# Kernel optimization log

Hardware: AMD Instinct MI355X
Metric: run time of the kernel (lower is better)

## Reference

```python
import jax, jax.numpy as jnp
import numpy as np

B, C, F = 262144, 64, 256
N_ITERS = 8


def setup_inputs() -> dict:
    key = jax.random.key(0)
    ks = jax.random.split(key, 8)
    s = lambda fan_in: 1.0 / np.sqrt(fan_in)
    return {
        "y": jax.random.normal(ks[0], (B, C), jnp.float32),
        "log_det_jacobians": jnp.zeros((B,), jnp.float32),
        "v": jax.random.normal(ks[1], (B, 1, C), jnp.float32),
        "W1": jax.random.normal(ks[2], (F, C), jnp.float32) * s(C),
        "b1": jnp.zeros((F,), jnp.float32),
        "W2": jax.random.normal(ks[3], (F, F), jnp.float32) * s(F),
        "b2": jnp.zeros((F,), jnp.float32),
        "W3": jax.random.normal(ks[4], (C, F), jnp.float32) * s(F),
        "b3": jnp.zeros((C,), jnp.float32),
    }


def reference(y, log_det_jacobians, v, W1, b1, W2, b2, W3, b3):
    def mlp(t):
        h = jax.nn.elu(t)
        h = jax.nn.elu(h @ W1.T + b1)
        h = jax.nn.elu(h @ W2.T + b2)
        return h @ W3.T + b3  # [B, C]

    g_y, vjp_fn = jax.vjp(mlp, y)
    v0 = v[:, 0, :]  # n_samples = 1
    w = v0
    log_det = jnp.zeros((y.shape[0],), y.dtype)
    for k in range(1, N_ITERS + 1):
        w = vjp_fn(w)[0]              # w <- w @ J, J = dg/dy
        inner = jnp.einsum('bd,bd->b', w, v0)
        # torch code: add when (k+1) % 2 == 0 (k odd), subtract when k even
        log_det = log_det + (inner / k if (k + 1) % 2 == 0 else -inner / k)

    z = y + g_y
    return z, log_det_jacobians + log_det
```

## Files before the change

kernel.cpp:

```cpp
#include <hip/hip_runtime.h>

#define BN 262144

typedef short bf16x8 __attribute__((ext_vector_type(8)));
typedef float f32x4 __attribute__((ext_vector_type(4)));
typedef unsigned int u32x2 __attribute__((ext_vector_type(2)));

#define MFMA16(a,b,c) __builtin_amdgcn_mfma_f32_16x16x32_bf16((a),(b),(c),0,0,0)

__device__ __forceinline__ unsigned short f2bf(float f) {
  union { float f; unsigned int u; } x; x.f = f;
  unsigned int u = x.u + 0x7fffu + ((x.u >> 16) & 1u);
  return (unsigned short)(u >> 16);
}
__device__ __forceinline__ float bf2f(unsigned int h) {
  union { unsigned int u; float f; } x; x.u = h << 16;
  return x.f;
}
__device__ __forceinline__ unsigned pk2(float lo, float hi) {
  union { float f; unsigned int u; } a, b; a.f = lo; b.f = hi;
  return (a.u >> 16) | (b.u & 0xffff0000u);
}
__device__ __forceinline__ unsigned swz(int row) {
  return (((unsigned)(row & 7)) << 4) ^ (((unsigned)(row & 8)) << 2);
}

#define O_R1 0
#define O_R2 16384
#define O_R3 81920
#define O_R4 98304
#define O_R5 114688
#define O_R6 180224
#define N_WS 196608

__global__ void invres_prep(const float* __restrict__ W1, const float* __restrict__ W2,
                            const float* __restrict__ W3, unsigned short* __restrict__ wsb) {
  int idx = blockIdx.x * 256 + threadIdx.x;
  if (idx >= N_WS) return;
  int j = idx & 7;
  int lane = (idx >> 3) & 63;
  int nn = lane & 15, kn = (lane >> 4) * 8 + j;
  float val;
  if (idx < O_R2) {
    int g = idx >> 9; int s = g & 1; int ct = g >> 1;
    val = W1[(ct * 16 + nn) * 64 + (s * 32 + kn)];
  } else if (idx < O_R3) {
    int g = (idx - O_R2) >> 9; int s = g & 7; int ct = g >> 3;
    val = W2[(ct * 16 + nn) * 256 + (s * 32 + kn)];
  } else if (idx < O_R4) {
    int g = (idx - O_R3) >> 9; int s = g & 7; int ct = g >> 3;
    val = W3[(ct * 16 + nn) * 256 + (s * 32 + kn)];
  } else if (idx < O_R5) {
    int g = (idx - O_R4) >> 9; int s = g & 1; int ct = g >> 1;
    val = W3[(s * 32 + kn) * 256 + (ct * 16 + nn)];
  } else if (idx < O_R6) {
    int g = (idx - O_R5) >> 9; int s = g & 7; int ct = g >> 3;
    val = W2[(s * 32 + kn) * 256 + (ct * 16 + nn)];
  } else {
    int g = (idx - O_R6) >> 9; int s = g & 7; int ct = g >> 3;
    val = W1[(s * 32 + kn) * 64 + (ct * 16 + nn)];
  }
  wsb[idx] = f2bf(val);
}

#define L_WB  16384
#define L_D1  20480
#define L_D2  36864
#define L_LDP 53248
#define L_SIZE 53760

__global__ void __launch_bounds__(512, 6)
invres_main(const float* __restrict__ y, const float* __restrict__ ldj,
            const float* __restrict__ v, const float* __restrict__ b1,
            const float* __restrict__ b2, const float* __restrict__ b3,
            const unsigned short* __restrict__ wsb, float* __restrict__ out) {
  extern __shared__ char smem[];
  char* P  = smem;
  char* WB = smem + L_WB;
  char* D1 = smem + L_D1;
  char* D2 = smem + L_D2;
  float* ldp = (float*)(smem + L_LDP);

  const int tid = threadIdx.x;
  const int lane = tid & 63;
  const int wid = tid >> 6;
  const int l15 = lane & 15, g16 = lane >> 4;
  const int ct0 = wid * 2;
  const int mh = wid >> 2;
  const int ctn = wid & 3;
  const int r0 = blockIdx.x * 32;

  const bf16x8* R1 = (const bf16x8*)(wsb + O_R1);
  const bf16x8* R2 = (const bf16x8*)(wsb + O_R2);
  const bf16x8* R3 = (const bf16x8*)(wsb + O_R3);
  const bf16x8* R4 = (const bf16x8*)(wsb + O_R4);
  const bf16x8* R5 = (const bf16x8*)(wsb + O_R5);
  const bf16x8* R6 = (const bf16x8*)(wsb + O_R6);

  auto mOff = [&](int mc) -> int { return ((wid * 4 + mc) * 64 + lane) * 8; };

  auto ldsA = [&](const char* buf, int mm, int s) -> bf16x8 {
    int row = mm * 16 + l15;
    unsigned byte = ((unsigned)(s * 64 + g16 * 16)) ^ swz(row);
    return *(const bf16x8*)(buf + row * 512 + byte);
  };
  auto stage64 = [&](char* buf, int mm, int cc, const float* hv) {
    int row = mm * 16 + l15;
    unsigned byte = ((unsigned)(((ct0 + cc) * 16 + g16 * 4) * 2)) ^ swz(row);
    u32x2 w; w[0] = pk2(hv[0], hv[1]); w[1] = pk2(hv[2], hv[3]);
    *(u32x2*)(buf + row * 512 + byte) = w;
  };
  auto gA = [&](const float* p, int mm, int s, bool elu) -> bf16x8 {
    const float* q = p + (size_t)(r0 + mm * 16 + l15) * 64 + s * 32 + g16 * 8;
    f32x4 a = __builtin_nontemporal_load((const f32x4*)q);
    f32x4 b = __builtin_nontemporal_load((const f32x4*)(q + 4));
    float xv[8] = {a[0], a[1], a[2], a[3], b[0], b[1], b[2], b[3]};
    bf16x8 f;
#pragma unroll
    for (int i = 0; i < 8; i++) {
      float x = xv[i];
      if (elu) x = x > 0.f ? x : (__expf(x) - 1.f);
      f[i] = (short)f2bf(x);
    }
    return f;
  };

  unsigned d0p[2], v0p[2];
  float ldacc[4] = {0.f, 0.f, 0.f, 0.f};

  {
    f32x4 bv1[2];
#pragma unroll
    for (int cc = 0; cc < 2; cc++) bv1[cc] = *(const f32x4*)(b1 + (ct0 + cc) * 16 + g16 * 4);
    f32x4 acc[2][2] = {};
#pragma unroll
    for (int s = 0; s < 2; s++) {
      bf16x8 a0 = gA(y, 0, s, true);
      bf16x8 a1 = gA(y, 1, s, true);
#pragma unroll
      for (int cc = 0; cc < 2; cc++) {
        bf16x8 B = R1[((ct0 + cc) * 2 + s) * 64 + lane];
        acc[0][cc] = MFMA16(B, a0, acc[0][cc]);
        acc[1][cc] = MFMA16(B, a1, acc[1][cc]);
      }
    }
#pragma unroll
    for (int mm = 0; mm < 2; mm++)
#pragma unroll
      for (int cc = 0; cc < 2; cc++) {
        float hv[4], dv[4];
#pragma unroll
        for (int r = 0; r < 4; r++) {
          float a = acc[mm][cc][r] + bv1[cc][r];
          float e = __expf(a);
          hv[r] = a > 0.f ? a : (e - 1.f);
          dv[r] = a > 0.f ? 1.f : e;
        }
        stage64(P, mm, cc, hv);
        u32x2 w; w[0] = pk2(dv[0], dv[1]); w[1] = pk2(dv[2], dv[3]);
        *(u32x2*)(D1 + mOff(mm * 2 + cc)) = w;
      }
  }
  __syncthreads();

  {
    f32x4 acc[2][2] = {};
#pragma unroll 1
    for (int s = 0; s < 8; s++) {
      bf16x8 a0 = ldsA(P, 0, s);
      bf16x8 a1 = ldsA(P, 1, s);
      bf16x8 B0 = R2[(ct0 * 8 + s) * 64 + lane];
      bf16x8 B1 = R2[((ct0 + 1) * 8 + s) * 64 + lane];
      acc[0][0] = MFMA16(B0, a0, acc[0][0]);
      acc[0][1] = MFMA16(B1, a0, acc[0][1]);
      acc[1][0] = MFMA16(B0, a1, acc[1][0]);
      acc[1][1] = MFMA16(B1, a1, acc[1][1]);
    }
    __syncthreads();
    f32x4 bv2[2];
#pragma unroll
    for (int cc = 0; cc < 2; cc++) bv2[cc] = *(const f32x4*)(b2 + (ct0 + cc) * 16 + g16 * 4);
#pragma unroll
    for (int mm = 0; mm < 2; mm++)
#pragma unroll
      for (int cc = 0; cc < 2; cc++) {
        float hv[4], dv[4];
#pragma unroll
        for (int r = 0; r < 4; r++) {
          float a = acc[mm][cc][r] + bv2[cc][r];
          float e = __expf(a);
          hv[r] = a > 0.f ? a : (e - 1.f);
          dv[r] = a > 0.f ? 1.f : e;
        }
        stage64(P, mm, cc, hv);
        u32x2 w; w[0] = pk2(dv[0], dv[1]); w[1] = pk2(dv[2], dv[3]);
        *(u32x2*)(D2 + mOff(mm * 2 + cc)) = w;
      }
  }
  __syncthreads();

  {
    f32x4 acc0 = {}, acc1 = {};
#pragma unroll 1
    for (int s = 0; s < 8; s += 2) {
      acc0 = MFMA16(R3[(ctn * 8 + s) * 64 + lane], ldsA(P, mh, s), acc0);
      acc1 = MFMA16(R3[(ctn * 8 + s + 1) * 64 + lane], ldsA(P, mh, s + 1), acc1);
    }
    f32x4 bv3 = *(const f32x4*)(b3 + ctn * 16 + g16 * 4);
    int row = r0 + mh * 16 + l15;
    int col = ctn * 16 + g16 * 4;
    size_t off = (size_t)row * 64 + col;
    f32x4 yv = __builtin_nontemporal_load((const f32x4*)(y + off));
    f32x4 vv = __builtin_nontemporal_load((const f32x4*)(v + off));
    f32x4 zv;
    float d0v[4];
#pragma unroll
    for (int r = 0; r < 4; r++) {
      zv[r] = yv[r] + acc0[r] + acc1[r] + bv3[r];
      d0v[r] = yv[r] > 0.f ? 1.f : __expf(yv[r]);
    }
    __builtin_nontemporal_store(zv, (f32x4*)(out + off));
    d0p[0] = pk2(d0v[0], d0v[1]); d0p[1] = pk2(d0v[2], d0v[3]);
    v0p[0] = pk2(vv[0], vv[1]);   v0p[1] = pk2(vv[2], vv[3]);
  }
  __syncthreads();

  {
    f32x4 acc[2][2] = {};
#pragma unroll
    for (int s = 0; s < 2; s++) {
      bf16x8 a0 = gA(v, 0, s, false);
      bf16x8 a1 = gA(v, 1, s, false);
#pragma unroll
      for (int cc = 0; cc < 2; cc++) {
        bf16x8 B = R4[((ct0 + cc) * 2 + s) * 64 + lane];
        acc[0][cc] = MFMA16(B, a0, acc[0][cc]);
        acc[1][cc] = MFMA16(B, a1, acc[1][cc]);
      }
    }
#pragma unroll
    for (int mm = 0; mm < 2; mm++)
#pragma unroll
      for (int cc = 0; cc < 2; cc++) {
        u32x2 dd = *(const u32x2*)(D2 + mOff(mm * 2 + cc));
        float uv[4];
#pragma unroll
        for (int r = 0; r < 4; r++)
          uv[r] = acc[mm][cc][r] * bf2f((dd[r >> 1] >> ((r & 1) * 16)) & 0xffffu);
        stage64(P, mm, cc, uv);
      }
  }
  __syncthreads();

  for (int k = 1; k <= 8; ++k) {
    {
      f32x4 acc[2][2] = {};
#pragma unroll 1
      for (int s = 0; s < 8; s++) {
        bf16x8 a0 = ldsA(P, 0, s);
        bf16x8 a1 = ldsA(P, 1, s);
        bf16x8 B0 = R5[(ct0 * 8 + s) * 64 + lane];
        bf16x8 B1 = R5[((ct0 + 1) * 8 + s) * 64 + lane];
        acc[0][0] = MFMA16(B0, a0, acc[0][0]);
        acc[0][1] = MFMA16(B1, a0, acc[0][1]);
        acc[1][0] = MFMA16(B0, a1, acc[1][0]);
        acc[1][1] = MFMA16(B1, a1, acc[1][1]);
      }
      __syncthreads();
#pragma unroll
      for (int mm = 0; mm < 2; mm++)
#pragma unroll
        for (int cc = 0; cc < 2; cc++) {
          u32x2 dd = *(const u32x2*)(D1 + mOff(mm * 2 + cc));
          float uv[4];
#pragma unroll
          for (int r = 0; r < 4; r++)
            uv[r] = acc[mm][cc][r] * bf2f((dd[r >> 1] >> ((r & 1) * 16)) & 0xffffu);
          stage64(P, mm, cc, uv);
        }
    }
    __syncthreads();

    {
      float coef = (k & 1) ? (1.f / (float)k) : (-1.f / (float)k);
      f32x4 acc0 = {}, acc1 = {};
#pragma unroll 1
      for (int s = 0; s < 8; s += 2) {
        acc0 = MFMA16(R6[(ctn * 8 + s) * 64 + lane], ldsA(P, mh, s), acc0);
        acc1 = MFMA16(R6[(ctn * 8 + s + 1) * 64 + lane], ldsA(P, mh, s + 1), acc1);
      }
      float wv[4];
#pragma unroll
      for (int r = 0; r < 4; r++) {
        wv[r] = (acc0[r] + acc1[r]) * bf2f((d0p[r >> 1] >> ((r & 1) * 16)) & 0xffffu);
        ldacc[r] += coef * wv[r] * bf2f((v0p[r >> 1] >> ((r & 1) * 16)) & 0xffffu);
      }
      if (k < 8) {
        int row = mh * 16 + l15;
        unsigned byte = ((unsigned)((ctn * 16 + g16 * 4) * 2)) ^ swz(row);
        u32x2 w; w[0] = pk2(wv[0], wv[1]); w[1] = pk2(wv[2], wv[3]);
        *(u32x2*)(WB + row * 128 + byte) = w;
      }
    }
    if (k < 8) {
      __syncthreads();
      f32x4 acc[2][2] = {};
#pragma unroll
      for (int s = 0; s < 2; s++) {
        bf16x8 a0, a1;
#pragma unroll
        for (int mm = 0; mm < 2; mm++) {
          int row = mm * 16 + l15;
          unsigned byte = ((unsigned)(s * 64 + g16 * 16)) ^ swz(row);
          bf16x8 a = *(const bf16x8*)(WB + row * 128 + byte);
          if (mm == 0) a0 = a; else a1 = a;
        }
#pragma unroll
        for (int cc = 0; cc < 2; cc++) {
          bf16x8 B = R4[((ct0 + cc) * 2 + s) * 64 + lane];
          acc[0][cc] = MFMA16(B, a0, acc[0][cc]);
          acc[1][cc] = MFMA16(B, a1, acc[1][cc]);
        }
      }
#pragma unroll
      for (int mm = 0; mm < 2; mm++)
#pragma unroll
        for (int cc = 0; cc < 2; cc++) {
          u32x2 dd = *(const u32x2*)(D2 + mOff(mm * 2 + cc));
          float uv[4];
#pragma unroll
          for (int r = 0; r < 4; r++)
            uv[r] = acc[mm][cc][r] * bf2f((dd[r >> 1] >> ((r & 1) * 16)) & 0xffffu);
          stage64(P, mm, cc, uv);
        }
      __syncthreads();
    }
  }

  {
    float s = ldacc[0] + ldacc[1] + ldacc[2] + ldacc[3];
    s += __shfl_xor(s, 16);
    s += __shfl_xor(s, 32);
    if (g16 == 0) ldp[(mh * 16 + l15) * 4 + ctn] = s;
  }
  __syncthreads();
  if (tid < 32) {
    float s = ldp[tid * 4] + ldp[tid * 4 + 1] + ldp[tid * 4 + 2] + ldp[tid * 4 + 3];
    int gb = r0 + tid;
    __builtin_nontemporal_store(ldj[gb] + s, out + (size_t)BN * 64 + gb);
  }
}

extern "C" void kernel_launch(void* const* d_in, const int* in_sizes, int n_in,
                              void* d_out, int out_size, void* d_ws, size_t ws_size,
                              hipStream_t stream) {
  const float* y   = (const float*)d_in[0];
  const float* ldj = (const float*)d_in[1];
  const float* v   = (const float*)d_in[2];
  const float* W1  = (const float*)d_in[3];
  const float* b1  = (const float*)d_in[4];
  const float* W2  = (const float*)d_in[5];
  const float* b2  = (const float*)d_in[6];
  const float* W3  = (const float*)d_in[7];
  const float* b3  = (const float*)d_in[8];
  unsigned short* wsb = (unsigned short*)d_ws;
  float* out = (float*)d_out;

  (void)hipFuncSetAttribute(reinterpret_cast<const void*>(&invres_main),
                            hipFuncAttributeMaxDynamicSharedMemorySize, L_SIZE);

  invres_prep<<<N_WS / 256, 256, 0, stream>>>(W1, W2, W3, wsb);
  invres_main<<<BN / 32, 512, L_SIZE, stream>>>(y, ldj, v, b1, b2, b3, wsb, out);
}
```

Before: 781.6 us.

## Double-buffer LDS activations and keep ELU derivatives in registers

Replaces the single LDS activation buffer with two ping-pong buffers, PA and PB, so each GEMM reads one buffer while writing the other. This removes the __syncthreads that sat between the MFMA loop and the staging writes in several stages. The bf16-packed ELU derivative masks D1 and D2 move from LDS into per-thread registers (16 extra VGPRs), which removes their LDS traffic and shrinks shared memory use. The cost is more register pressure under launch bounds of 512 threads with 6 blocks, which could force spills.

Measured after the change: 1.376 ms. 1.76x slower.

```diff
diff --git a/kernel.cpp b/kernel.cpp
--- a/kernel.cpp
+++ b/kernel.cpp
@@ -63,11 +63,10 @@
   wsb[idx] = f2bf(val);
 }
 
-#define L_WB  16384
-#define L_D1  20480
-#define L_D2  36864
-#define L_LDP 53248
-#define L_SIZE 53760
+#define L_PB  16384
+#define L_WB  32768
+#define L_LDP 36864
+#define L_SIZE 37376
 
 __global__ void __launch_bounds__(512, 6)
 invres_main(const float* __restrict__ y, const float* __restrict__ ldj,
@@ -75,10 +74,9 @@
             const float* __restrict__ b2, const float* __restrict__ b3,
             const unsigned short* __restrict__ wsb, float* __restrict__ out) {
   extern __shared__ char smem[];
-  char* P  = smem;
+  char* PA = smem;
+  char* PB = smem + L_PB;
   char* WB = smem + L_WB;
-  char* D1 = smem + L_D1;
-  char* D2 = smem + L_D2;
   float* ldp = (float*)(smem + L_LDP);
 
   const int tid = threadIdx.x;
@@ -96,8 +94,6 @@
   const bf16x8* R4 = (const bf16x8*)(wsb + O_R4);
   const bf16x8* R5 = (const bf16x8*)(wsb + O_R5);
   const bf16x8* R6 = (const bf16x8*)(wsb + O_R6);
-
-  auto mOff = [&](int mc) -> int { return ((wid * 4 + mc) * 64 + lane) * 8; };
 
   auto ldsA = [&](const char* buf, int mm, int s) -> bf16x8 {
     int row = mm * 16 + l15;
@@ -125,7 +121,7 @@
     return f;
   };
 
-  unsigned d0p[2], v0p[2];
+  unsigned d1p[8], d2p[8], d0p[2], v0p[2];
   float ldacc[4] = {0.f, 0.f, 0.f, 0.f};
 
   {
@@ -156,9 +152,10 @@
           hv[r] = a > 0.f ? a : (e - 1.f);
           dv[r] = a > 0.f ? 1.f : e;
         }
-        stage64(P, mm, cc, hv);
-        u32x2 w; w[0] = pk2(dv[0], dv[1]); w[1] = pk2(dv[2], dv[3]);
-        *(u32x2*)(D1 + mOff(mm * 2 + cc)) = w;
+        stage64(PA, mm, cc, hv);
+        int base = (mm * 2 + cc) * 2;
+        d1p[base] = pk2(dv[0], dv[1]);
+        d1p[base + 1] = pk2(dv[2], dv[3]);
       }
   }
   __syncthreads();
@@ -167,8 +164,8 @@
     f32x4 acc[2][2] = {};
 #pragma unroll 1
     for (int s = 0; s < 8; s++) {
-      bf16x8 a0 = ldsA(P, 0, s);
-      bf16x8 a1 = ldsA(P, 1, s);
+      bf16x8 a0 = ldsA(PA, 0, s);
+      bf16x8 a1 = ldsA(PA, 1, s);
       bf16x8 B0 = R2[(ct0 * 8 + s) * 64 + lane];
       bf16x8 B1 = R2[((ct0 + 1) * 8 + s) * 64 + lane];
       acc[0][0] = MFMA16(B0, a0, acc[0][0]);
@@ -176,7 +173,6 @@
       acc[1][0] = MFMA16(B0, a1, acc[1][0]);
       acc[1][1] = MFMA16(B1, a1, acc[1][1]);
     }
-    __syncthreads();
     f32x4 bv2[2];
 #pragma unroll
     for (int cc = 0; cc < 2; cc++) bv2[cc] = *(const f32x4*)(b2 + (ct0 + cc) * 16 + g16 * 4);
@@ -192,9 +188,10 @@
           hv[r] = a > 0.f ? a : (e - 1.f);
           dv[r] = a > 0.f ? 1.f : e;
         }
-        stage64(P, mm, cc, hv);
-        u32x2 w; w[0] = pk2(dv[0], dv[1]); w[1] = pk2(dv[2], dv[3]);
-        *(u32x2*)(D2 + mOff(mm * 2 + cc)) = w;
+        stage64(PB, mm, cc, hv);
+        int base = (mm * 2 + cc) * 2;
+        d2p[base] = pk2(dv[0], dv[1]);
+        d2p[base + 1] = pk2(dv[2], dv[3]);
       }
   }
   __syncthreads();
@@ -203,8 +200,8 @@
     f32x4 acc0 = {}, acc1 = {};
 #pragma unroll 1
     for (int s = 0; s < 8; s += 2) {
-      acc0 = MFMA16(R3[(ctn * 8 + s) * 64 + lane], ldsA(P, mh, s), acc0);
-      acc1 = MFMA16(R3[(ctn * 8 + s + 1) * 64 + lane], ldsA(P, mh, s + 1), acc1);
+      acc0 = MFMA16(R3[(ctn * 8 + s) * 64 + lane], ldsA(PB, mh, s), acc0);
+      acc1 = MFMA16(R3[(ctn * 8 + s + 1) * 64 + lane], ldsA(PB, mh, s + 1), acc1);
     }
     f32x4 bv3 = *(const f32x4*)(b3 + ctn * 16 + g16 * 4);
     int row = r0 + mh * 16 + l15;
@@ -223,7 +220,6 @@
     d0p[0] = pk2(d0v[0], d0v[1]); d0p[1] = pk2(d0v[2], d0v[3]);
     v0p[0] = pk2(vv[0], vv[1]);   v0p[1] = pk2(vv[2], vv[3]);
   }
-  __syncthreads();
 
   {
     f32x4 acc[2][2] = {};
@@ -242,12 +238,12 @@
     for (int mm = 0; mm < 2; mm++)
 #pragma unroll
       for (int cc = 0; cc < 2; cc++) {
-        u32x2 dd = *(const u32x2*)(D2 + mOff(mm * 2 + cc));
+        int base = (mm * 2 + cc) * 2;
         float uv[4];
 #pragma unroll
         for (int r = 0; r < 4; r++)
-          uv[r] = acc[mm][cc][r] * bf2f((dd[r >> 1] >> ((r & 1) * 16)) & 0xffffu);
-        stage64(P, mm, cc, uv);
+          uv[r] = acc[mm][cc][r] * bf2f((d2p[base + (r >> 1)] >> ((r & 1) * 16)) & 0xffffu);
+        stage64(PA, mm, cc, uv);
       }
   }
   __syncthreads();
@@ -257,8 +253,8 @@
       f32x4 acc[2][2] = {};
 #pragma unroll 1
       for (int s = 0; s < 8; s++) {
-        bf16x8 a0 = ldsA(P, 0, s);
-        bf16x8 a1 = ldsA(P, 1, s);
+        bf16x8 a0 = ldsA(PA, 0, s);
+        bf16x8 a1 = ldsA(PA, 1, s);
         bf16x8 B0 = R5[(ct0 * 8 + s) * 64 + lane];
         bf16x8 B1 = R5[((ct0 + 1) * 8 + s) * 64 + lane];
         acc[0][0] = MFMA16(B0, a0, acc[0][0]);
@@ -266,17 +262,16 @@
         acc[1][0] = MFMA16(B0, a1, acc[1][0]);
         acc[1][1] = MFMA16(B1, a1, acc[1][1]);
       }
-      __syncthreads();
 #pragma unroll
       for (int mm = 0; mm < 2; mm++)
 #pragma unroll
         for (int cc = 0; cc < 2; cc++) {
-          u32x2 dd = *(const u32x2*)(D1 + mOff(mm * 2 + cc));
+          int base = (mm * 2 + cc) * 2;
           float uv[4];
 #pragma unroll
           for (int r = 0; r < 4; r++)
-            uv[r] = acc[mm][cc][r] * bf2f((dd[r >> 1] >> ((r & 1) * 16)) & 0xffffu);
-          stage64(P, mm, cc, uv);
+            uv[r] = acc[mm][cc][r] * bf2f((d1p[base + (r >> 1)] >> ((r & 1) * 16)) & 0xffffu);
+          stage64(PB, mm, cc, uv);
         }
     }
     __syncthreads();
@@ -286,8 +281,8 @@
       f32x4 acc0 = {}, acc1 = {};
 #pragma unroll 1
       for (int s = 0; s < 8; s += 2) {
-        acc0 = MFMA16(R6[(ctn * 8 + s) * 64 + lane], ldsA(P, mh, s), acc0);
-        acc1 = MFMA16(R6[(ctn * 8 + s + 1) * 64 + lane], ldsA(P, mh, s + 1), acc1);
+        acc0 = MFMA16(R6[(ctn * 8 + s) * 64 + lane], ldsA(PB, mh, s), acc0);
+        acc1 = MFMA16(R6[(ctn * 8 + s + 1) * 64 + lane], ldsA(PB, mh, s + 1), acc1);
       }
       float wv[4];
 #pragma unroll
@@ -326,12 +321,12 @@
       for (int mm = 0; mm < 2; mm++)
 #pragma unroll
         for (int cc = 0; cc < 2; cc++) {
-          u32x2 dd = *(const u32x2*)(D2 + mOff(mm * 2 + cc));
+          int base = (mm * 2 + cc) * 2;
           float uv[4];
 #pragma unroll
           for (int r = 0; r < 4; r++)
-            uv[r] = acc[mm][cc][r] * bf2f((dd[r >> 1] >> ((r & 1) * 16)) & 0xffffu);
-          stage64(P, mm, cc, uv);
+            uv[r] = acc[mm][cc][r] * bf2f((d2p[base + (r >> 1)] >> ((r & 1) * 16)) & 0xffffu);
+          stage64(PA, mm, cc, uv);
         }
       __syncthreads();
     }
```
